# Performance work log

Hardware: AMD Instinct MI355X
Metric: run time of the kernel (lower is better)

The kernel has to match this reference:

```python
import jax, jax.numpy as jnp
import numpy as np

BH, S, D = 32, 2048, 128

def setup_inputs() -> dict:
    key = jax.random.key(0)
    k1, k2, k3 = jax.random.split(key, 3)
    return {
        "key": jax.random.normal(k1, (BH, S, D), dtype=jnp.float32),
        "query": jax.random.normal(k2, (BH, S, D), dtype=jnp.float32),
        "value": jax.random.normal(k3, (BH, S, D), dtype=jnp.float32),
    }

def reference(key, query, value):
    # scores = Q K^T / sqrt(d)  -> softmax over keys -> @ V
    scale = 1.0 / np.sqrt(key.shape[-1]).astype(np.float32)
    scores = jnp.einsum('bqd,bkd->bqk', query, key) * scale  # [BH, S, S]
    probs = jax.nn.softmax(scores, axis=-1)
    return jnp.einsum('bqk,bkd->bqd', probs, value)  # [BH, S, D]
```

## Files before the change

### kernel.cpp

```cpp
#include <hip/hip_runtime.h>
#include <hip/hip_bf16.h>
#include <cmath>

#define BH_N 32
#define SEQ  2048
#define DH   128
#define BM   256
#define KT   64
#define NTILES (SEQ / KT)

typedef __attribute__((ext_vector_type(4)))  float f32x4;
typedef __attribute__((ext_vector_type(16))) float f32x16;
typedef __attribute__((ext_vector_type(8)))  short bf16x8;
typedef __attribute__((ext_vector_type(4)))  unsigned int u32x4;

__device__ __forceinline__ unsigned cvtpk(float lo, float hi) {
  unsigned r;
  asm("v_cvt_pk_bf16_f32 %0, %1, %2" : "=v"(r) : "v"(lo), "v"(hi));
  return r;
}


__global__ __launch_bounds__(512, 2) void attn_fwd(
    const float* __restrict__ Kg, const float* __restrict__ Qg,
    const float* __restrict__ Vg, float* __restrict__ Og)
{
  __shared__ __align__(16) char lds[65536];
  constexpr float QSC = 0.08838834764831845f * 1.4426950408889634f;

  const int t    = threadIdx.x;
  const int lane = t & 63;
  const int w    = t >> 6;
  const int hi   = lane >> 5;
  const int q31  = lane & 31;

  const int bid = blockIdx.x;
  const int lb  = (bid & 7) * 32 + (bid >> 3);
  const int bh  = lb >> 3;
  const int qb  = lb & 7;
  const int blkq = qb * BM;
  const size_t base = (size_t)bh * SEQ * DH;

  bf16x8 qf[8];
  {
    const float* qp = Qg + base + (size_t)(blkq + w * 32 + q31) * DH + hi * 8;
    #pragma unroll
    for (int s = 0; s < 8; ++s) {
      const float4 a = *(const float4*)(qp + s * 16);
      const float4 b = *(const float4*)(qp + s * 16 + 4);
      u32x4 u = { cvtpk(a.x * QSC, a.y * QSC), cvtpk(a.z * QSC, a.w * QSC),
                  cvtpk(b.x * QSC, b.y * QSC), cvtpk(b.z * QSC, b.w * QSC) };
      qf[s] = __builtin_bit_cast(bf16x8, u);
    }
  }

  const int kq = t >> 4;
  const int kd = (t & 15) * 8;
  const int vd = t & 127;
  const int vk = (t >> 7) * 16;
  const float* kp0 = Kg + base + (size_t)kq * DH + kd;
  const float* vp0 = Vg + base + (size_t)vk * DH + vd;

  auto kv_load = [&](int tile2, float4* kf4, float* vv) {
    const float* kp = kp0 + (size_t)tile2 * (KT * DH);
    kf4[0] = *(const float4*)kp;
    kf4[1] = *(const float4*)(kp + 4);
    kf4[2] = *(const float4*)(kp + 32 * DH);
    kf4[3] = *(const float4*)(kp + 32 * DH + 4);
    const float* vp = vp0 + (size_t)tile2 * (KT * DH);
    #pragma unroll
    for (int j = 0; j < 16; ++j) vv[j] = vp[j * DH];
  };
  auto kv_write = [&](char* bb, const float4* kf4, const float* vv) {
    #pragma unroll
    for (int i = 0; i < 2; ++i) {
      const int key = kq + i * 32;
      u32x4 u = { cvtpk(kf4[2*i].x, kf4[2*i].y), cvtpk(kf4[2*i].z, kf4[2*i].w),
                  cvtpk(kf4[2*i+1].x, kf4[2*i+1].y), cvtpk(kf4[2*i+1].z, kf4[2*i+1].w) };
      *(u32x4*)(bb + key * 256 + ((kd * 2) ^ ((key & 15) << 4))) = u;
    }
    u32x4 u0 = { cvtpk(vv[0], vv[1]),  cvtpk(vv[2], vv[3]),
                 cvtpk(vv[4], vv[5]),  cvtpk(vv[6], vv[7]) };
    u32x4 u1 = { cvtpk(vv[8], vv[9]),  cvtpk(vv[10], vv[11]),
                 cvtpk(vv[12], vv[13]), cvtpk(vv[14], vv[15]) };
    const int vsw = (vd & 7) << 4;
    *(u32x4*)(bb + 16384 + vd * 128 + ((vk * 2) ^ vsw)) = u0;
    *(u32x4*)(bb + 16384 + vd * 128 + ((vk * 2 + 16) ^ vsw)) = u1;
  };

  f32x16 ot[4];
  #pragma unroll
  for (int dt = 0; dt < 4; ++dt)
    #pragma unroll
    for (int r = 0; r < 16; ++r) ot[dt][r] = 0.f;

  float m_run = -INFINITY;
  float l_run = 0.f;

  {
    float4 kf4[4]; float vv[16];
    kv_load(0, kf4, vv);
    kv_write(lds, kf4, vv);
  }
  __syncthreads();

  for (int tile = 0; tile < NTILES; ++tile) {
    char* cbp = lds + (tile & 1) * 32768;
    float4 kf4[4]; float vv[16];
    const bool pre = (tile + 1 < NTILES);
    if (pre) kv_load(tile + 1, kf4, vv);

    f32x16 st[2];
    #pragma unroll
    for (int kt = 0; kt < 2; ++kt)
      #pragma unroll
      for (int r = 0; r < 16; ++r) st[kt][r] = 0.f;
    #pragma unroll
    for (int kt = 0; kt < 2; ++kt) {
      const int row = kt * 32 + q31;
      const int ksw = (row & 15) << 4;
      char* rb = cbp + row * 256;
      #pragma unroll
      for (int ks = 0; ks < 8; ++ks) {
        const bf16x8 kf = *(const bf16x8*)(rb + ((ks * 32 + hi * 16) ^ ksw));
        st[kt] = __builtin_amdgcn_mfma_f32_32x32x16_bf16(kf, qf[ks], st[kt], 0, 0, 0);
      }
    }

    float tm = st[0][0];
    #pragma unroll
    for (int kt = 0; kt < 2; ++kt)
      #pragma unroll
      for (int r = 0; r < 16; ++r) tm = fmaxf(tm, st[kt][r]);
    tm = fmaxf(tm, __shfl_xor(tm, 32));
    if (!__all(tm <= m_run + 8.0f)) {
      const float mnew = fmaxf(m_run, tm);
      const float rs   = exp2f(m_run - mnew);
      l_run *= rs;
      #pragma unroll
      for (int dt = 0; dt < 4; ++dt)
        #pragma unroll
        for (int r = 0; r < 16; ++r) ot[dt][r] *= rs;
      m_run = mnew;
    }
    float psum = 0.f;
    #pragma unroll
    for (int kt = 0; kt < 2; ++kt)
      #pragma unroll
      for (int r = 0; r < 16; ++r) {
        const float p = exp2f(st[kt][r] - m_run);
        st[kt][r] = p;
        psum += p;
      }
    psum += __shfl_xor(psum, 32);
    l_run += psum;

    bf16x8 pf[4];
    #pragma unroll
    for (int kt = 0; kt < 2; ++kt) {
      unsigned a0 = cvtpk(st[kt][0], st[kt][1]);
      unsigned b0 = cvtpk(st[kt][4], st[kt][5]);
      asm volatile("v_permlane32_swap_b32 %0, %1" : "+v"(a0), "+v"(b0));
      unsigned c0 = cvtpk(st[kt][2], st[kt][3]);
      unsigned d0 = cvtpk(st[kt][6], st[kt][7]);
      asm volatile("v_permlane32_swap_b32 %0, %1" : "+v"(c0), "+v"(d0));
      u32x4 ue = { a0, c0, b0, d0 };
      pf[2 * kt] = __builtin_bit_cast(bf16x8, ue);
      unsigned a1 = cvtpk(st[kt][8],  st[kt][9]);
      unsigned b1 = cvtpk(st[kt][12], st[kt][13]);
      asm volatile("v_permlane32_swap_b32 %0, %1" : "+v"(a1), "+v"(b1));
      unsigned c1 = cvtpk(st[kt][10], st[kt][11]);
      unsigned d1 = cvtpk(st[kt][14], st[kt][15]);
      asm volatile("v_permlane32_swap_b32 %0, %1" : "+v"(c1), "+v"(d1));
      u32x4 uo = { a1, c1, b1, d1 };
      pf[2 * kt + 1] = __builtin_bit_cast(bf16x8, uo);
    }

    #pragma unroll
    for (int ks = 0; ks < 4; ++ks)
      #pragma unroll
      for (int dt = 0; dt < 4; ++dt) {
        const int row = dt * 32 + q31;
        const bf16x8 vf = *(const bf16x8*)(cbp + 16384 + row * 128 +
                                           ((ks * 32 + hi * 16) ^ ((row & 7) << 4)));
        ot[dt] = __builtin_amdgcn_mfma_f32_32x32x16_bf16(vf, pf[ks], ot[dt], 0, 0, 0);
      }

    if (pre) kv_write(lds + ((tile + 1) & 1) * 32768, kf4, vv);
    __syncthreads();
  }

  const float rcp = 1.0f / l_run;
  char* ep = lds + (w << 12);
  const int qsw = (q31 & 7) << 4;
  const int qr  = lane >> 1;
  const int hf  = lane & 1;
  const int rsw = (qr & 7) << 4;
  float* orow = Og + base + (size_t)(blkq + w * 32) * DH;
  #pragma unroll
  for (int dt = 0; dt < 4; ++dt) {
    #pragma unroll
    for (int a = 0; a < 4; ++a) {
      f32x4 v = { ot[dt][4*a+0] * rcp, ot[dt][4*a+1] * rcp,
                  ot[dt][4*a+2] * rcp, ot[dt][4*a+3] * rcp };
      const int dl = 8 * a + 4 * hi;
      *(f32x4*)(ep + q31 * 128 + ((dl * 4) ^ qsw)) = v;
    }
    float* op = orow + (size_t)qr * DH + dt * 32 + hf * 16;
    #pragma unroll
    for (int u = 0; u < 4; ++u) {
      const f32x4 v = *(const f32x4*)(ep + qr * 128 + ((hf * 64 + u * 16) ^ rsw));
      *(f32x4*)(op + u * 4) = v;
    }
    __syncthreads();
  }
}

extern "C" void kernel_launch(void* const* d_in, const int* in_sizes, int n_in,
                              void* d_out, int out_size, void* d_ws, size_t ws_size,
                              hipStream_t stream) {
  const float* Kg = (const float*)d_in[0];
  const float* Qg = (const float*)d_in[1];
  const float* Vg = (const float*)d_in[2];
  float* Og = (float*)d_out;
  attn_fwd<<<dim3(BH_N * (SEQ / BM)), dim3(512), 0, stream>>>(Kg, Qg, Vg, Og);
}
```

Measured before the change: 105.0 us.

## Double the KV tile and interleave QK and PV halves with split K/V prefetch

Raises the key tile from 64 to 128 and doubles the LDS buffers to 128 KB. Each tile is processed as two 64-key halves, with the second half's QK^T MFMAs issued alongside the first half's PV MFMAs. K and V prefetch loads and LDS writes are split and spread through the loop. V is now loaded with float4 global reads and stored in a transposed, XOR-swizzled 256-byte-row layout, and s_setprio is raised around the MFMA blocks. The aim is fewer barriers per key and better overlap of memory, exp and matrix work, at the cost of more registers and LDS use that allows only one block per CU.

New measurement: 101.4 us. -3.4%, faster.

```diff
diff --git a/kernel.cpp b/kernel.cpp
--- a/kernel.cpp
+++ b/kernel.cpp
@@ -6,7 +6,7 @@
 #define SEQ  2048
 #define DH   128
 #define BM   256
-#define KT   64
+#define KT   128
 #define NTILES (SEQ / KT)
 
 typedef __attribute__((ext_vector_type(4)))  float f32x4;
@@ -25,7 +25,7 @@
     const float* __restrict__ Kg, const float* __restrict__ Qg,
     const float* __restrict__ Vg, float* __restrict__ Og)
 {
-  __shared__ __align__(16) char lds[65536];
+  __shared__ __align__(16) char lds[131072];
   constexpr float QSC = 0.08838834764831845f * 1.4426950408889634f;
 
   const int t    = threadIdx.x;
@@ -54,38 +54,45 @@
     }
   }
 
-  const int kq = t >> 4;
-  const int kd = (t & 15) * 8;
-  const int vd = t & 127;
-  const int vk = (t >> 7) * 16;
+  const int kq  = t >> 4;
+  const int kd  = (t & 15) * 8;
+  const int vd4 = (t & 31) * 4;
+  const int vk8 = (t >> 5) * 8;
   const float* kp0 = Kg + base + (size_t)kq * DH + kd;
-  const float* vp0 = Vg + base + (size_t)vk * DH + vd;
-
-  auto kv_load = [&](int tile2, float4* kf4, float* vv) {
-    const float* kp = kp0 + (size_t)tile2 * (KT * DH);
-    kf4[0] = *(const float4*)kp;
-    kf4[1] = *(const float4*)(kp + 4);
-    kf4[2] = *(const float4*)(kp + 32 * DH);
-    kf4[3] = *(const float4*)(kp + 32 * DH + 4);
-    const float* vp = vp0 + (size_t)tile2 * (KT * DH);
-    #pragma unroll
-    for (int j = 0; j < 16; ++j) vv[j] = vp[j * DH];
-  };
-  auto kv_write = [&](char* bb, const float4* kf4, const float* vv) {
-    #pragma unroll
-    for (int i = 0; i < 2; ++i) {
+  const float* vp0 = Vg + base + (size_t)vk8 * DH + vd4;
+
+  auto k_load = [&](int tile, float4* kf4) {
+    const float* kp = kp0 + (size_t)tile * (KT * DH);
+    #pragma unroll
+    for (int i = 0; i < 4; ++i) {
+      kf4[2*i]   = *(const float4*)(kp + (size_t)i * 32 * DH);
+      kf4[2*i+1] = *(const float4*)(kp + (size_t)i * 32 * DH + 4);
+    }
+  };
+  auto k_write = [&](char* bb, const float4* kf4) {
+    #pragma unroll
+    for (int i = 0; i < 4; ++i) {
       const int key = kq + i * 32;
-      u32x4 u = { cvtpk(kf4[2*i].x, kf4[2*i].y), cvtpk(kf4[2*i].z, kf4[2*i].w),
+      u32x4 u = { cvtpk(kf4[2*i].x, kf4[2*i].y),   cvtpk(kf4[2*i].z, kf4[2*i].w),
                   cvtpk(kf4[2*i+1].x, kf4[2*i+1].y), cvtpk(kf4[2*i+1].z, kf4[2*i+1].w) };
       *(u32x4*)(bb + key * 256 + ((kd * 2) ^ ((key & 15) << 4))) = u;
     }
-    u32x4 u0 = { cvtpk(vv[0], vv[1]),  cvtpk(vv[2], vv[3]),
-                 cvtpk(vv[4], vv[5]),  cvtpk(vv[6], vv[7]) };
-    u32x4 u1 = { cvtpk(vv[8], vv[9]),  cvtpk(vv[10], vv[11]),
-                 cvtpk(vv[12], vv[13]), cvtpk(vv[14], vv[15]) };
-    const int vsw = (vd & 7) << 4;
-    *(u32x4*)(bb + 16384 + vd * 128 + ((vk * 2) ^ vsw)) = u0;
-    *(u32x4*)(bb + 16384 + vd * 128 + ((vk * 2 + 16) ^ vsw)) = u1;
+  };
+  auto v_load = [&](int tile, float4* vv4) {
+    const float* vp = vp0 + (size_t)tile * (KT * DH);
+    #pragma unroll
+    for (int j = 0; j < 8; ++j) vv4[j] = *(const float4*)(vp + (size_t)j * DH);
+  };
+  auto v_write = [&](char* bb, const float4* vv4) {
+    #pragma unroll
+    for (int r = 0; r < 4; ++r) {
+      const int row = vd4 + r;
+      const float* f = (const float*)vv4;
+      u32x4 u = { cvtpk(vv4[0][r], vv4[1][r]), cvtpk(vv4[2][r], vv4[3][r]),
+                  cvtpk(vv4[4][r], vv4[5][r]), cvtpk(vv4[6][r], vv4[7][r]) };
+      (void)f;
+      *(u32x4*)(bb + 32768 + row * 256 + ((vk8 * 2) ^ ((row & 15) << 4))) = u;
+    }
   };
 
   f32x16 ot[4];
@@ -98,35 +105,36 @@
   float l_run = 0.f;
 
   {
-    float4 kf4[4]; float vv[16];
-    kv_load(0, kf4, vv);
-    kv_write(lds, kf4, vv);
+    float4 kf4[8], vv4[8];
+    k_load(0, kf4); v_load(0, vv4);
+    k_write(lds, kf4); v_write(lds, vv4);
   }
   __syncthreads();
 
-  for (int tile = 0; tile < NTILES; ++tile) {
-    char* cbp = lds + (tile & 1) * 32768;
-    float4 kf4[4]; float vv[16];
-    const bool pre = (tile + 1 < NTILES);
-    if (pre) kv_load(tile + 1, kf4, vv);
-
-    f32x16 st[2];
+  f32x16 st[2];
+  bf16x8 pfA[4], pfB[4];
+
+  auto qk_pass = [&](const char* cbp, int krow0) {
     #pragma unroll
     for (int kt = 0; kt < 2; ++kt)
       #pragma unroll
       for (int r = 0; r < 16; ++r) st[kt][r] = 0.f;
+    __builtin_amdgcn_s_setprio(1);
     #pragma unroll
     for (int kt = 0; kt < 2; ++kt) {
-      const int row = kt * 32 + q31;
+      const int row = krow0 + kt * 32 + q31;
       const int ksw = (row & 15) << 4;
-      char* rb = cbp + row * 256;
+      const char* rb = cbp + row * 256;
       #pragma unroll
       for (int ks = 0; ks < 8; ++ks) {
         const bf16x8 kf = *(const bf16x8*)(rb + ((ks * 32 + hi * 16) ^ ksw));
         st[kt] = __builtin_amdgcn_mfma_f32_32x32x16_bf16(kf, qf[ks], st[kt], 0, 0, 0);
       }
     }
-
+    __builtin_amdgcn_s_setprio(0);
+  };
+
+  auto softmax_pack = [&](bf16x8* pf) {
     float tm = st[0][0];
     #pragma unroll
     for (int kt = 0; kt < 2; ++kt)
@@ -154,8 +162,6 @@
       }
     psum += __shfl_xor(psum, 32);
     l_run += psum;
-
-    bf16x8 pf[4];
     #pragma unroll
     for (int kt = 0; kt < 2; ++kt) {
       unsigned a0 = cvtpk(st[kt][0], st[kt][1]);
@@ -175,18 +181,38 @@
       u32x4 uo = { a1, c1, b1, d1 };
       pf[2 * kt + 1] = __builtin_bit_cast(bf16x8, uo);
     }
-
+  };
+
+  auto pv_pass = [&](const char* cbp, int ks0, const bf16x8* pf) {
+    __builtin_amdgcn_s_setprio(1);
     #pragma unroll
     for (int ks = 0; ks < 4; ++ks)
       #pragma unroll
       for (int dt = 0; dt < 4; ++dt) {
         const int row = dt * 32 + q31;
-        const bf16x8 vf = *(const bf16x8*)(cbp + 16384 + row * 128 +
-                                           ((ks * 32 + hi * 16) ^ ((row & 7) << 4)));
+        const bf16x8 vf = *(const bf16x8*)(cbp + 32768 + row * 256 +
+                                           (((ks0 + ks) * 32 + hi * 16) ^ ((row & 15) << 4)));
         ot[dt] = __builtin_amdgcn_mfma_f32_32x32x16_bf16(vf, pf[ks], ot[dt], 0, 0, 0);
       }
-
-    if (pre) kv_write(lds + ((tile + 1) & 1) * 32768, kf4, vv);
+    __builtin_amdgcn_s_setprio(0);
+  };
+
+  for (int tile = 0; tile < NTILES; ++tile) {
+    char* cbp = lds + (tile & 1) * 65536;
+    char* nbp = lds + ((tile + 1) & 1) * 65536;
+    const bool pre = (tile + 1 < NTILES);
+    float4 kf4[8], vv4[8];
+
+    if (pre) k_load(tile + 1, kf4);
+    qk_pass(cbp, 0);
+    softmax_pack(pfA);
+    if (pre) k_write(nbp, kf4);
+    if (pre) v_load(tile + 1, vv4);
+    qk_pass(cbp, 64);
+    pv_pass(cbp, 0, pfA);
+    softmax_pack(pfB);
+    if (pre) v_write(nbp, vv4);
+    pv_pass(cbp, 4, pfB);
     __syncthreads();
   }
 
```
